# Performance work log

Hardware: AMD Instinct MI355X
Metric: run time of the kernel (lower is better)

Reference implementation:

```python
import jax, jax.numpy as jnp
import numpy as np

DIM = 2048
K_DIM = 2048
Q_HEADS = 16
KV_HEADS = 4
HEAD_DIM = DIM // Q_HEADS  # 128
KV_DIM = HEAD_DIM * KV_HEADS  # 512
MAX_LEN = 2048
ROPE_THETA = 10000.0
ROPE_FACTOR = 8.0


def _rope_cos_sin(seq_len):
    # Faithful to generate_sin_cos_pos_emb with is_causal=True
    d = HEAD_DIM
    seq_eff = max(seq_len, MAX_LEN)
    base_adj = (ROPE_FACTOR * seq_eff / MAX_LEN - (ROPE_FACTOR - 1.0)) ** (d / (d - 2))
    adjusted_base = ROPE_THETA * base_adj
    inv_freq = 1.0 / adjusted_base ** (np.arange(0, d, 2, dtype=np.float32) / d)
    pos = np.arange(seq_len, dtype=np.float32)  # causal: no centering
    freqs = pos[:, None] * inv_freq[None, :]            # [S, d/2]
    emb = np.concatenate([freqs, freqs], axis=-1)        # [S, d]
    return jnp.asarray(np.cos(emb), jnp.float32), jnp.asarray(np.sin(emb), jnp.float32)


def _rotate_half(x):
    x1, x2 = jnp.split(x, 2, axis=-1)
    return jnp.concatenate([-x2, x1], axis=-1)


def setup_inputs() -> dict:
    key = jax.random.key(0)
    ks = jax.random.split(key, 12)
    B, S = 1, 2048
    s_in = 1.0 / np.sqrt(DIM)
    s_k = 1.0 / np.sqrt(K_DIM)
    return {
        "query": jax.random.normal(ks[0], (B, S, DIM), jnp.float32),
        "key": jax.random.normal(ks[1], (B, S, K_DIM), jnp.float32),
        "value": jax.random.normal(ks[2], (B, S, K_DIM), jnp.float32),
        "Wq": jax.random.uniform(ks[3], (DIM, DIM), jnp.float32, -s_in, s_in),
        "bq": jax.random.uniform(ks[4], (DIM,), jnp.float32, -s_in, s_in),
        "Wk": jax.random.uniform(ks[5], (KV_DIM, K_DIM), jnp.float32, -s_k, s_k),
        "bk": jax.random.uniform(ks[6], (KV_DIM,), jnp.float32, -s_k, s_k),
        "Wv": jax.random.uniform(ks[7], (KV_DIM, K_DIM), jnp.float32, -s_k, s_k),
        "bv": jax.random.uniform(ks[8], (KV_DIM,), jnp.float32, -s_k, s_k),
        "Wo": jax.random.uniform(ks[9], (DIM, DIM), jnp.float32, -s_in, s_in),
        "bo": jax.random.uniform(ks[10], (DIM,), jnp.float32, -s_in, s_in),
    }


def reference(query, key, value, Wq, bq, Wk, bk, Wv, bv, Wo, bo):
    B, S, _ = query.shape
    scale = HEAD_DIM ** -0.5

    q = query @ Wq.T + bq                                   # [B,S,DIM]
    k = key @ Wk.T + bk                                     # [B,S,KV_DIM]
    v = value @ Wv.T + bv                                   # [B,S,KV_DIM]

    q = q.reshape(B, S, Q_HEADS, HEAD_DIM)
    k = k.reshape(B, S, KV_HEADS, HEAD_DIM)
    v = v.reshape(B, S, KV_HEADS, HEAD_DIM)

    cos, sin = _rope_cos_sin(S)                              # [S,D]
    cos = cos[None, :, None, :]
    sin = sin[None, :, None, :]
    q = q * cos + _rotate_half(q) * sin
    k = k * cos + _rotate_half(k) * sin

    # [B,H,S,D]
    q = q.transpose(0, 2, 1, 3)
    k = k.transpose(0, 2, 1, 3)
    v = v.transpose(0, 2, 1, 3)

    rep = Q_HEADS // KV_HEADS
    k = jnp.repeat(k, rep, axis=1)
    v = jnp.repeat(v, rep, axis=1)

    scores = jnp.einsum('bhqd,bhkd->bhqk', q, k) * scale
    causal = jnp.tril(jnp.ones((S, S), bool))
    scores = jnp.where(causal[None, None], scores, jnp.finfo(scores.dtype).min)
    attn = jax.nn.softmax(scores, axis=-1)
    out = jnp.einsum('bhqk,bhkd->bhqd', attn, v)             # [B,H,S,D]

    out = out.transpose(0, 2, 1, 3).reshape(B, S, DIM)
    return out @ Wo.T + bo
```

## Files before the change

kernel.cpp:

```cpp
#include <hip/hip_runtime.h>
#include <stdint.h>

typedef __attribute__((ext_vector_type(8))) short short8;
typedef __attribute__((ext_vector_type(4))) float f32x4;
typedef __attribute__((ext_vector_type(4))) unsigned short u16x4;
typedef unsigned short bf16_t;

__device__ __forceinline__ bf16_t f2bf(float f) {
  union { float f; uint32_t u; } x; x.f = f;
  uint32_t r = x.u + 0x7fffu + ((x.u >> 16) & 1u);
  return (bf16_t)(r >> 16);
}

__device__ __forceinline__ void ld_g2l_16(const bf16_t* g, bf16_t* l) {
  __builtin_amdgcn_global_load_lds(
      (const __attribute__((address_space(1))) void*)g,
      (__attribute__((address_space(3))) void*)l, 16, 0, 0);
}

__global__ void convert_all(const float* __restrict__ s0, const float* __restrict__ s1,
                            const float* __restrict__ s2, const float* __restrict__ s3,
                            const float* __restrict__ s4, const float* __restrict__ s5,
                            const float* __restrict__ s6,
                            bf16_t* __restrict__ d0, bf16_t* __restrict__ d1,
                            bf16_t* __restrict__ d2, bf16_t* __restrict__ d3,
                            bf16_t* __restrict__ d4, bf16_t* __restrict__ d5,
                            bf16_t* __restrict__ d6,
                            float* __restrict__ CS, float* __restrict__ SN) {
  int i = blockIdx.x * 256 + threadIdx.x;
  if (i < 131072) {
    int fi = i & 63, pos = i >> 6;
    float ang = (float)pos * exp2f((float)fi * -0.2076205059f);
    CS[i] = cosf(ang);
    SN[i] = sinf(ang);
  }
  const float* src; bf16_t* dst; int off;
  if (i < 5 * 1048576) {
    int t = i >> 20; off = i & 1048575;
    if (t == 0)      { src = s0; dst = d0; }
    else if (t == 1) { src = s1; dst = d1; }
    else if (t == 2) { src = s2; dst = d2; }
    else if (t == 3) { src = s3; dst = d3; }
    else             { src = s4; dst = d4; }
  } else {
    int j = i - 5 * 1048576;
    if (j < 262144) { src = s5; dst = d5; off = j; }
    else            { src = s6; dst = d6; off = j - 262144; }
  }
  f32x4 v = *(const f32x4*)(src + (size_t)off * 4);
  u16x4 o;
  o[0] = f2bf(v[0]); o[1] = f2bf(v[1]); o[2] = f2bf(v[2]); o[3] = f2bf(v[3]);
  *(u16x4*)(dst + (size_t)off * 4) = o;
}

template <int MODE>
__device__ __forceinline__ void gemm_core(
    bf16_t* __restrict__ As, bf16_t* __restrict__ Bs,
    const bf16_t* __restrict__ A, const bf16_t* __restrict__ Bm,
    const float* __restrict__ bias, void* __restrict__ Cout,
    int N, int K, int m0, int n0,
    const float* __restrict__ CS, const float* __restrict__ SN) {
  const int tid = threadIdx.x;
  const int lane = tid & 63, quad = lane >> 4, l16 = lane & 15;
  const int wv = tid >> 6;
  const int wr = wv >> 1, wc = wv & 1;
  const int swz = (l16 & 7) << 3;

  f32x4 acc[2][4];
  const f32x4 zf = {0.f, 0.f, 0.f, 0.f};
#pragma unroll
  for (int mi = 0; mi < 2; ++mi)
#pragma unroll
    for (int ni = 0; ni < 4; ++ni) acc[mi][ni] = zf;

  const int rT = tid >> 3;
  const int colsw = (((tid & 7) ^ (rT & 7)) << 3);
  const bf16_t* Ap0 = A + (size_t)(m0 + rT) * K + colsw;
  const bf16_t* Ap1 = A + (size_t)(m0 + rT + 32) * K + colsw;
  const bf16_t* Bp0 = Bm + (size_t)(n0 + rT) * K + colsw;
  const bf16_t* Bp1 = Bm + (size_t)(n0 + rT + 32) * K + colsw;
  const bf16_t* Bp2 = Bm + (size_t)(n0 + rT + 64) * K + colsw;
  const bf16_t* Bp3 = Bm + (size_t)(n0 + rT + 96) * K + colsw;

  auto STAGE = [&](int buf, int k0) {
    ld_g2l_16(Ap0 + k0, As + buf * 4096 + tid * 8);
    ld_g2l_16(Ap1 + k0, As + buf * 4096 + (tid + 256) * 8);
    ld_g2l_16(Bp0 + k0, Bs + buf * 8192 + tid * 8);
    ld_g2l_16(Bp1 + k0, Bs + buf * 8192 + (tid + 256) * 8);
    ld_g2l_16(Bp2 + k0, Bs + buf * 8192 + (tid + 512) * 8);
    ld_g2l_16(Bp3 + k0, Bs + buf * 8192 + (tid + 768) * 8);
  };

  STAGE(0, 0);
  __syncthreads();
  int buf = 0;

  for (int k0 = 0; k0 < K; k0 += 64) {
    if (k0 + 64 < K) STAGE(buf ^ 1, k0 + 64);
    const bf16_t* Ab = As + buf * 4096;
    const bf16_t* Bb = Bs + buf * 8192;
    short8 af[2][2], bfv[4][2];
#pragma unroll
    for (int mi = 0; mi < 2; ++mi) {
      int rowL = wr * 32 + mi * 16 + l16;
#pragma unroll
      for (int kc = 0; kc < 2; ++kc)
        af[mi][kc] = *(const short8*)(
            &Ab[rowL * 64 + ((kc * 32 + quad * 8) ^ swz)]);
    }
#pragma unroll
    for (int ni = 0; ni < 4; ++ni) {
      int rowB = wc * 32 + (ni & 1) * 16 + (ni >> 1) * 64 + l16;
#pragma unroll
      for (int kc = 0; kc < 2; ++kc)
        bfv[ni][kc] = *(const short8*)(
            &Bb[rowB * 64 + ((kc * 32 + quad * 8) ^ swz)]);
    }
#pragma unroll
    for (int kc = 0; kc < 2; ++kc)
#pragma unroll
      for (int mi = 0; mi < 2; ++mi)
#pragma unroll
        for (int ni = 0; ni < 4; ++ni)
          acc[mi][ni] = __builtin_amdgcn_mfma_f32_16x16x32_bf16(
              af[mi][kc], bfv[ni][kc], acc[mi][ni], 0, 0, 0);
    __asm__ volatile("s_waitcnt vmcnt(0)" ::: "memory");
    __syncthreads();
    buf ^= 1;
  }

  if (MODE == 0 || MODE == 2) {
#pragma unroll
    for (int mi = 0; mi < 2; ++mi)
#pragma unroll
      for (int ni = 0; ni < 4; ++ni) {
        int n = n0 + wc * 32 + (ni & 1) * 16 + (ni >> 1) * 64 + l16;
        int mbase = m0 + wr * 32 + mi * 16 + quad * 4;
        float bv = bias[n];
#pragma unroll
        for (int r = 0; r < 4; ++r) {
          float v = acc[mi][ni][r] + bv;
          int m = mbase + r;
          if (MODE == 0) ((float*)Cout)[(size_t)m * N + n] = v;
          else           ((bf16_t*)Cout)[(size_t)n * 2048 + m] = f2bf(v);
        }
      }
  } else {
    const float scale = (MODE == 3) ? 0.12751744f : 1.0f;
    bf16_t* dst = (bf16_t*)Cout;
#pragma unroll
    for (int mi = 0; mi < 2; ++mi)
#pragma unroll
      for (int r = 0; r < 4; ++r) {
        int m = m0 + wr * 32 + mi * 16 + quad * 4 + r;
#pragma unroll
        for (int ni = 0; ni < 2; ++ni) {
          int i = wc * 32 + ni * 16 + l16;
          int n_lo = n0 + i;
          float v1 = acc[mi][ni][r] + bias[n_lo];
          float v2 = acc[mi][ni + 2][r] + bias[n_lo + 64];
          float c = CS[m * 64 + i];
          float s = SN[m * 64 + i];
          float o1 = (v1 * c - v2 * s) * scale;
          float o2 = (v2 * c + v1 * s) * scale;
          dst[(size_t)m * N + n_lo] = f2bf(o1);
          dst[(size_t)m * N + n_lo + 64] = f2bf(o2);
        }
      }
  }
}

__global__ __launch_bounds__(256) void gemm_qkv(
    const bf16_t* __restrict__ qb, const bf16_t* __restrict__ kb,
    const bf16_t* __restrict__ vb, const bf16_t* __restrict__ wqb,
    const bf16_t* __restrict__ wkb, const bf16_t* __restrict__ wvb,
    const float* __restrict__ bq, const float* __restrict__ bk,
    const float* __restrict__ bv, bf16_t* __restrict__ Qr,
    bf16_t* __restrict__ Kr, bf16_t* __restrict__ Vt,
    const float* __restrict__ CS, const float* __restrict__ SN) {
  __shared__ __align__(16) bf16_t As[2 * 64 * 64];
  __shared__ __align__(16) bf16_t Bs[2 * 128 * 64];
  int bid = blockIdx.x;
  int job = (bid & 7) * 96 + (bid >> 3);
  int bx = job >> 5, m0 = (job & 31) * 64;
  if (bx < 16)
    gemm_core<3>(As, Bs, qb, wqb, bq, Qr, 2048, 2048, m0, bx * 128, CS, SN);
  else if (bx < 20)
    gemm_core<4>(As, Bs, kb, wkb, bk, Kr, 512, 2048, m0, (bx - 16) * 128, CS, SN);
  else
    gemm_core<2>(As, Bs, vb, wvb, bv, Vt, 512, 2048, m0, (bx - 20) * 128, CS, SN);
}

__global__ __launch_bounds__(256) void gemm_o(
    const bf16_t* __restrict__ Ob, const bf16_t* __restrict__ wob,
    const float* __restrict__ bo, float* __restrict__ out) {
  __shared__ __align__(16) bf16_t As[2 * 64 * 64];
  __shared__ __align__(16) bf16_t Bs[2 * 128 * 64];
  int bid = blockIdx.x;
  int job = (bid & 7) * 64 + (bid >> 3);
  int bx = job >> 5, m0 = (job & 31) * 64;
  gemm_core<0>(As, Bs, Ob, wob, bo, out, 2048, 2048, m0, bx * 128,
               nullptr, nullptr);
}

__global__ __launch_bounds__(256, 2) void attn_fwd(
    const bf16_t* __restrict__ Qr, const bf16_t* __restrict__ Kr,
    const bf16_t* __restrict__ Vt, bf16_t* __restrict__ Oo) {
  const int h = blockIdx.y;
  const int bx = blockIdx.x;
  const int qt = (h < 8) ? (31 - bx) : bx;
  const int T = qt + 1;

  const int tid = threadIdx.x;
  const int wv = tid >> 6, lane = tid & 63, quad = lane >> 4, l16 = lane & 15;
  const int q_base = qt * 64 + wv * 16;
  const int hkv = h >> 2;
  const int qg = q_base + l16;
  const int swzE = (l16 & 7) << 3;

  __shared__ __align__(16) bf16_t Ks[2][64 * 128];
  __shared__ __align__(16) bf16_t Vs[2][128 * 64];

  short8 qf[4];
  {
    const bf16_t* qp = Qr + (size_t)qg * 2048 + h * 128 + quad * 8;
#pragma unroll
    for (int kc = 0; kc < 4; ++kc) qf[kc] = *(const short8*)(qp + kc * 32);
  }

  const f32x4 zf = {0.f, 0.f, 0.f, 0.f};
  f32x4 o[8];
#pragma unroll
  for (int di = 0; di < 8; ++di) o[di] = zf;
  float l_acc = 0.f;

  auto STAGE = [&](int buf, int t) {
    const int k0 = t * 64;
    bf16_t* KB = &Ks[buf][0];
    bf16_t* VB = &Vs[buf][0];
#pragma unroll
    for (int m = 0; m < 4; ++m) {
      int rK = wv * 16 + m * 4 + (lane >> 4);
      const bf16_t* gK = Kr + (size_t)(k0 + rK) * 512 + hkv * 128
                         + (((lane & 15) ^ ((4 * (m & 1)) | quad)) << 3);
      ld_g2l_16(gK, KB + rK * 128 + ((lane & 15) << 3));
      int rV = wv * 32 + m * 8 + (lane >> 3);
      const bf16_t* gV = Vt + (size_t)(hkv * 128 + rV) * 2048 + k0
                         + (((lane & 7) ^ ((lane >> 3) & 7)) << 3);
      ld_g2l_16(gV, VB + rV * 64 + ((lane & 7) << 3));
    }
  };

  STAGE(0, 0);
  __syncthreads();
  int buf = 0;

  for (int t = 0; t < T; ++t) {
    if (t + 1 < T) STAGE(buf ^ 1, t + 1);
    const bf16_t* KB = &Ks[buf][0];
    const bf16_t* VB = &Vs[buf][0];
    const int k0 = t * 64;

    f32x4 sacc[4];
#pragma unroll
    for (int sub = 0; sub < 4; ++sub) sacc[sub] = zf;
#pragma unroll
    for (int sub = 0; sub < 4; ++sub)
#pragma unroll
      for (int kc = 0; kc < 4; ++kc) {
        short8 kf = *(const short8*)(
            &KB[(sub * 16 + l16) * 128 + ((kc * 32 + quad * 8) ^ swzE)]);
        sacc[sub] = __builtin_amdgcn_mfma_f32_16x16x32_bf16(kf, qf[kc], sacc[sub], 0, 0, 0);
      }

    const bool dg = (k0 + 63 > q_base);
    uint32_t Dw[4][2];
#pragma unroll
    for (int sub = 0; sub < 4; ++sub) {
      float pv[4];
#pragma unroll
      for (int r = 0; r < 4; ++r) {
        float e = exp2f(sacc[sub][r]);
        if (dg) {
          int kg = k0 + sub * 16 + quad * 4 + r;
          if (kg > qg) e = 0.f;
        }
        pv[r] = e;
        l_acc += e;
      }
      asm("v_cvt_pk_bf16_f32 %0, %1, %2" : "=v"(Dw[sub][0]) : "v"(pv[0]), "v"(pv[1]));
      asm("v_cvt_pk_bf16_f32 %0, %1, %2" : "=v"(Dw[sub][1]) : "v"(pv[2]), "v"(pv[3]));
    }

    const int aA = ((((quad * 2) & 3) << 4) + l16) << 2;
    const int aB = ((((quad * 2 + 1) & 3) << 4) + l16) << 2;
    const bool losel = quad < 2;
#define BPERM(a, x) ((uint32_t)__builtin_amdgcn_ds_bpermute((a), (int)(x)))
    union { uint32_t w[4]; short8 v; } U0, U1;
    {
      uint32_t t0, t1;
      t0 = BPERM(aA, Dw[0][0]); t1 = BPERM(aA, Dw[1][0]); U0.w[0] = losel ? t0 : t1;
      t0 = BPERM(aA, Dw[0][1]); t1 = BPERM(aA, Dw[1][1]); U0.w[1] = losel ? t0 : t1;
      t0 = BPERM(aB, Dw[0][0]); t1 = BPERM(aB, Dw[1][0]); U0.w[2] = losel ? t0 : t1;
      t0 = BPERM(aB, Dw[0][1]); t1 = BPERM(aB, Dw[1][1]); U0.w[3] = losel ? t0 : t1;
      t0 = BPERM(aA, Dw[2][0]); t1 = BPERM(aA, Dw[3][0]); U1.w[0] = losel ? t0 : t1;
      t0 = BPERM(aA, Dw[2][1]); t1 = BPERM(aA, Dw[3][1]); U1.w[1] = losel ? t0 : t1;
      t0 = BPERM(aB, Dw[2][0]); t1 = BPERM(aB, Dw[3][0]); U1.w[2] = losel ? t0 : t1;
      t0 = BPERM(aB, Dw[2][1]); t1 = BPERM(aB, Dw[3][1]); U1.w[3] = losel ? t0 : t1;
    }
#undef BPERM
    const short8 pf0 = U0.v, pf1 = U1.v;

#pragma unroll
    for (int di = 0; di < 8; ++di) {
      short8 vf0 = *(const short8*)(
          &VB[(di * 16 + l16) * 64 + ((quad * 8) ^ swzE)]);
      short8 vf1 = *(const short8*)(
          &VB[(di * 16 + l16) * 64 + ((quad * 8 + 32) ^ swzE)]);
      o[di] = __builtin_amdgcn_mfma_f32_16x16x32_bf16(pf0, vf0, o[di], 0, 0, 0);
      o[di] = __builtin_amdgcn_mfma_f32_16x16x32_bf16(pf1, vf1, o[di], 0, 0, 0);
    }

    __asm__ volatile("s_waitcnt vmcnt(0)" ::: "memory");
    __syncthreads();
    buf ^= 1;
  }

  float lf = l_acc;
  lf += __shfl_xor(lf, 16);
  lf += __shfl_xor(lf, 32);
  float linv[4];
#pragma unroll
  for (int r = 0; r < 4; ++r) linv[r] = 1.0f / __shfl(lf, quad * 4 + r, 64);
#pragma unroll
  for (int di = 0; di < 8; ++di)
#pragma unroll
    for (int r = 0; r < 4; ++r) {
      size_t row = q_base + quad * 4 + r;
      size_t col = h * 128 + di * 16 + l16;
      Oo[row * 2048 + col] = f2bf(o[di][r] * linv[r]);
    }
}

extern "C" void kernel_launch(void* const* d_in, const int* in_sizes, int n_in,
                              void* d_out, int out_size, void* d_ws, size_t ws_size,
                              hipStream_t stream) {
  (void)in_sizes; (void)n_in; (void)out_size; (void)ws_size;
  const float* query = (const float*)d_in[0];
  const float* key = (const float*)d_in[1];
  const float* value = (const float*)d_in[2];
  const float* Wq = (const float*)d_in[3];
  const float* bq = (const float*)d_in[4];
  const float* Wk = (const float*)d_in[5];
  const float* bk = (const float*)d_in[6];
  const float* Wv = (const float*)d_in[7];
  const float* bv = (const float*)d_in[8];
  const float* Wo = (const float*)d_in[9];
  const float* bo = (const float*)d_in[10];
  float* out = (float*)d_out;

  char* ws = (char*)d_ws;
  const size_t MB = 1024 * 1024;
  bf16_t* qb  = (bf16_t*)(ws + 0 * MB);
  bf16_t* kb  = (bf16_t*)(ws + 8 * MB);
  bf16_t* vb  = (bf16_t*)(ws + 16 * MB);
  bf16_t* wqb = (bf16_t*)(ws + 24 * MB);
  bf16_t* wkb = (bf16_t*)(ws + 32 * MB);
  bf16_t* wvb = (bf16_t*)(ws + 34 * MB);
  bf16_t* wob = (bf16_t*)(ws + 36 * MB);
  bf16_t* Qr  = (bf16_t*)(ws + 44 * MB);
  bf16_t* Kr  = (bf16_t*)(ws + 52 * MB);
  bf16_t* Vt  = (bf16_t*)(ws + 54 * MB);
  bf16_t* Ob  = (bf16_t*)(ws + 56 * MB);
  float*  CS  = (float*)(ws + 64 * MB);
  float*  SN  = (float*)(ws + 64 * MB + 512 * 1024);

  convert_all<<<22528, 256, 0, stream>>>(query, key, value, Wq, Wo, Wk, Wv,
                                         qb, kb, vb, wqb, wob, wkb, wvb, CS, SN);
  gemm_qkv<<<768, 256, 0, stream>>>(qb, kb, vb, wqb, wkb, wvb,
                                    bq, bk, bv, Qr, Kr, Vt, CS, SN);
  attn_fwd<<<dim3(32, 16), 256, 0, stream>>>(Qr, Kr, Vt, Ob);
  gemm_o<<<512, 256, 0, stream>>>(Ob, wob, bo, out);
}
```

Baseline: 259.0 us.

## Split attention KV range across two blocks and merge partials in combine kernel

Each query tile's causal key range is now split into two halves, handled by separate blocks. This doubles the grid to 64x16, and each block writes unnormalized fp32 partial outputs and row sums. A new attn_combine kernel adds the partials, normalizes them and converts to bf16. The key/value tile shrinks from 64 to 32 rows and the launch bound asks for 4 blocks per CU, to raise occupancy and balance the load. The cost is an extra launch and about 32MB of fp32 partial traffic, written into workspace regions that held already-consumed inputs.

```diff
diff --git a/kernel.cpp b/kernel.cpp
--- a/kernel.cpp
+++ b/kernel.cpp
@@ -203,23 +203,31 @@
                nullptr, nullptr);
 }
 
-__global__ __launch_bounds__(256, 2) void attn_fwd(
+__global__ __launch_bounds__(256, 4) void attn_fwd(
     const bf16_t* __restrict__ Qr, const bf16_t* __restrict__ Kr,
-    const bf16_t* __restrict__ Vt, bf16_t* __restrict__ Oo) {
+    const bf16_t* __restrict__ Vt, float* __restrict__ Op0,
+    float* __restrict__ Op1, float* __restrict__ Lp0,
+    float* __restrict__ Lp1) {
   const int h = blockIdx.y;
   const int bx = blockIdx.x;
-  const int qt = (h < 8) ? (31 - bx) : bx;
-  const int T = qt + 1;
+  const int qt = 31 - (bx >> 1);
+  const int ch = bx & 1;
+  const int half = qt + 1;
+  const int t_beg = ch ? half : 0;
+  const int t_end = ch ? 2 * half : half;
+  float* __restrict__ Op = ch ? Op1 : Op0;
+  float* __restrict__ Lp = ch ? Lp1 : Lp0;
 
   const int tid = threadIdx.x;
   const int wv = tid >> 6, lane = tid & 63, quad = lane >> 4, l16 = lane & 15;
   const int q_base = qt * 64 + wv * 16;
   const int hkv = h >> 2;
   const int qg = q_base + l16;
-  const int swzE = (l16 & 7) << 3;
-
-  __shared__ __align__(16) bf16_t Ks[2][64 * 128];
-  __shared__ __align__(16) bf16_t Vs[2][128 * 64];
+  const int swzK = (l16 & 7) << 3;
+  const int swzV = (l16 & 3) << 3;
+
+  __shared__ __align__(16) bf16_t Ks[2][32 * 128];
+  __shared__ __align__(16) bf16_t Vs[2][128 * 32];
 
   short8 qf[4];
   {
@@ -235,48 +243,49 @@
   float l_acc = 0.f;
 
   auto STAGE = [&](int buf, int t) {
-    const int k0 = t * 64;
+    const int k0 = t * 32;
     bf16_t* KB = &Ks[buf][0];
     bf16_t* VB = &Vs[buf][0];
 #pragma unroll
-    for (int m = 0; m < 4; ++m) {
-      int rK = wv * 16 + m * 4 + (lane >> 4);
+    for (int j = 0; j < 2; ++j) {
+      int c = tid + j * 256;
+      int rK = c >> 4, c8 = c & 15;
       const bf16_t* gK = Kr + (size_t)(k0 + rK) * 512 + hkv * 128
-                         + (((lane & 15) ^ ((4 * (m & 1)) | quad)) << 3);
-      ld_g2l_16(gK, KB + rK * 128 + ((lane & 15) << 3));
-      int rV = wv * 32 + m * 8 + (lane >> 3);
-      const bf16_t* gV = Vt + (size_t)(hkv * 128 + rV) * 2048 + k0
-                         + (((lane & 7) ^ ((lane >> 3) & 7)) << 3);
-      ld_g2l_16(gV, VB + rV * 64 + ((lane & 7) << 3));
+                         + ((c8 ^ (rK & 7)) << 3);
+      ld_g2l_16(gK, KB + c * 8);
+      int dV = c >> 2, v8 = c & 3;
+      const bf16_t* gV = Vt + (size_t)(hkv * 128 + dV) * 2048 + k0
+                         + ((v8 ^ (dV & 3)) << 3);
+      ld_g2l_16(gV, VB + c * 8);
     }
   };
 
-  STAGE(0, 0);
+  STAGE(0, t_beg);
   __syncthreads();
   int buf = 0;
 
-  for (int t = 0; t < T; ++t) {
-    if (t + 1 < T) STAGE(buf ^ 1, t + 1);
+  for (int t = t_beg; t < t_end; ++t) {
+    if (t + 1 < t_end) STAGE(buf ^ 1, t + 1);
     const bf16_t* KB = &Ks[buf][0];
     const bf16_t* VB = &Vs[buf][0];
-    const int k0 = t * 64;
-
-    f32x4 sacc[4];
-#pragma unroll
-    for (int sub = 0; sub < 4; ++sub) sacc[sub] = zf;
-#pragma unroll
-    for (int sub = 0; sub < 4; ++sub)
+    const int k0 = t * 32;
+
+    f32x4 sacc[2];
+#pragma unroll
+    for (int sub = 0; sub < 2; ++sub) sacc[sub] = zf;
+#pragma unroll
+    for (int sub = 0; sub < 2; ++sub)
 #pragma unroll
       for (int kc = 0; kc < 4; ++kc) {
         short8 kf = *(const short8*)(
-            &KB[(sub * 16 + l16) * 128 + ((kc * 32 + quad * 8) ^ swzE)]);
+            &KB[(sub * 16 + l16) * 128 + ((kc * 32 + quad * 8) ^ swzK)]);
         sacc[sub] = __builtin_amdgcn_mfma_f32_16x16x32_bf16(kf, qf[kc], sacc[sub], 0, 0, 0);
       }
 
-    const bool dg = (k0 + 63 > q_base);
-    uint32_t Dw[4][2];
-#pragma unroll
-    for (int sub = 0; sub < 4; ++sub) {
+    const bool dg = (k0 + 31 > q_base);
+    uint32_t Dw[2][2];
+#pragma unroll
+    for (int sub = 0; sub < 2; ++sub) {
       float pv[4];
 #pragma unroll
       for (int r = 0; r < 4; ++r) {
@@ -296,30 +305,24 @@
     const int aB = ((((quad * 2 + 1) & 3) << 4) + l16) << 2;
     const bool losel = quad < 2;
 #define BPERM(a, x) ((uint32_t)__builtin_amdgcn_ds_bpermute((a), (int)(x)))
-    union { uint32_t w[4]; short8 v; } U0, U1;
+    union { uint32_t w[4]; short8 v; } U0;
     {
       uint32_t t0, t1;
       t0 = BPERM(aA, Dw[0][0]); t1 = BPERM(aA, Dw[1][0]); U0.w[0] = losel ? t0 : t1;
       t0 = BPERM(aA, Dw[0][1]); t1 = BPERM(aA, Dw[1][1]); U0.w[1] = losel ? t0 : t1;
       t0 = BPERM(aB, Dw[0][0]); t1 = BPERM(aB, Dw[1][0]); U0.w[2] = losel ? t0 : t1;
       t0 = BPERM(aB, Dw[0][1]); t1 = BPERM(aB, Dw[1][1]); U0.w[3] = losel ? t0 : t1;
-      t0 = BPERM(aA, Dw[2][0]); t1 = BPERM(aA, Dw[3][0]); U1.w[0] = losel ? t0 : t1;
-      t0 = BPERM(aA, Dw[2][1]); t1 = BPERM(aA, Dw[3][1]); U1.w[1] = losel ? t0 : t1;
-      t0 = BPERM(aB, Dw[2][0]); t1 = BPERM(aB, Dw[3][0]); U1.w[2] = losel ? t0 : t1;
-      t0 = BPERM(aB, Dw[2][1]); t1 = BPERM(aB, Dw[3][1]); U1.w[3] = losel ? t0 : t1;
     }
 #undef BPERM
-    const short8 pf0 = U0.v, pf1 = U1.v;
+    const short8 pf0 = U0.v;
 
 #pragma unroll
     for (int di = 0; di < 8; ++di) {
-      short8 vf0 = *(const short8*)(
-          &VB[(di * 16 + l16) * 64 + ((quad * 8) ^ swzE)]);
-      short8 vf1 = *(const short8*)(
-          &VB[(di * 16 + l16) * 64 + ((quad * 8 + 32) ^ swzE)]);
-      o[di] = __builtin_amdgcn_mfma_f32_16x16x32_bf16(pf0, vf0, o[di], 0, 0, 0);
-      o[di] = __builtin_amdgcn_mfma_f32_16x16x32_bf16(pf1, vf1, o[di], 0, 0, 0);
-    }
+      short8 vf = *(const short8*)(
+          &Vs[buf][(di * 16 + l16) * 32 + ((quad * 8) ^ swzV)]);
+      o[di] = __builtin_amdgcn_mfma_f32_16x16x32_bf16(pf0, vf, o[di], 0, 0, 0);
+    }
+    (void)VB;
 
     __asm__ volatile("s_waitcnt vmcnt(0)" ::: "memory");
     __syncthreads();
@@ -329,17 +332,39 @@
   float lf = l_acc;
   lf += __shfl_xor(lf, 16);
   lf += __shfl_xor(lf, 32);
-  float linv[4];
-#pragma unroll
-  for (int r = 0; r < 4; ++r) linv[r] = 1.0f / __shfl(lf, quad * 4 + r, 64);
+  if (quad == 0) Lp[(h << 11) + q_base + l16] = lf;
 #pragma unroll
   for (int di = 0; di < 8; ++di)
 #pragma unroll
     for (int r = 0; r < 4; ++r) {
       size_t row = q_base + quad * 4 + r;
       size_t col = h * 128 + di * 16 + l16;
-      Oo[row * 2048 + col] = f2bf(o[di][r] * linv[r]);
-    }
+      Op[row * 2048 + col] = o[di][r];
+    }
+}
+
+__global__ __launch_bounds__(256) void attn_combine(
+    const float* __restrict__ Op0, const float* __restrict__ Op1,
+    const float* __restrict__ Lp0, const float* __restrict__ Lp1,
+    bf16_t* __restrict__ Ob) {
+  int idx = blockIdx.x * 256 + threadIdx.x;
+  size_t base = (size_t)idx * 8;
+  int row = (int)(base >> 11);
+  int col = (int)(base & 2047);
+  int h = col >> 7;
+  float li = 1.0f / (Lp0[(h << 11) + row] + Lp1[(h << 11) + row]);
+  f32x4 a0 = *(const f32x4*)(Op0 + base);
+  f32x4 a1 = *(const f32x4*)(Op0 + base + 4);
+  f32x4 b0 = *(const f32x4*)(Op1 + base);
+  f32x4 b1 = *(const f32x4*)(Op1 + base + 4);
+  u16x4 o0, o1;
+#pragma unroll
+  for (int j = 0; j < 4; ++j) {
+    o0[j] = f2bf((a0[j] + b0[j]) * li);
+    o1[j] = f2bf((a1[j] + b1[j]) * li);
+  }
+  *(u16x4*)(Ob + base) = o0;
+  *(u16x4*)(Ob + base + 4) = o1;
 }
 
 extern "C" void kernel_launch(void* const* d_in, const int* in_sizes, int n_in,
@@ -375,10 +400,16 @@
   float*  CS  = (float*)(ws + 64 * MB);
   float*  SN  = (float*)(ws + 64 * MB + 512 * 1024);
 
+  float* Op0 = (float*)(ws + 0 * MB);
+  float* Op1 = (float*)(ws + 16 * MB);
+  float* Lp0 = (float*)(ws + 32 * MB);
+  float* Lp1 = (float*)(ws + 32 * MB + 256 * 1024);
+
   convert_all<<<22528, 256, 0, stream>>>(query, key, value, Wq, Wo, Wk, Wv,
                                          qb, kb, vb, wqb, wob, wkb, wvb, CS, SN);
   gemm_qkv<<<768, 256, 0, stream>>>(qb, kb, vb, wqb, wkb, wvb,
                                     bq, bk, bv, Qr, Kr, Vt, CS, SN);
-  attn_fwd<<<dim3(32, 16), 256, 0, stream>>>(Qr, Kr, Vt, Ob);
+  attn_fwd<<<dim3(64, 16), 256, 0, stream>>>(Qr, Kr, Vt, Op0, Op1, Lp0, Lp1);
+  attn_combine<<<2048, 256, 0, stream>>>(Op0, Op1, Lp0, Lp1, Ob);
   gemm_o<<<512, 256, 0, stream>>>(Ob, wob, bo, out);
 }
```

After: 275.8 us. 1.06x slower.
